# Optimization experiments

Measured on AMD Instinct MI355X. Metric: run time of the kernel, lower is better.

The kernel has to match this reference:

```python
import jax, jax.numpy as jnp
import numpy as np

N_NODES = 100000
N_EDGES = 3200000
IN_DIM, H_DIM, OUT_DIM = 512, 256, 128
NEG_SLOPE = 0.25


def setup_inputs() -> dict:
    key = jax.random.key(0)
    ks = jax.random.split(key, 8)
    x = jax.random.normal(ks[0], (N_NODES, IN_DIM), dtype=jnp.float32)
    # xavier-normal-ish init for weights, zero bias (matches module init)
    W1 = jax.random.normal(ks[1], (IN_DIM, H_DIM), dtype=jnp.float32) * np.sqrt(2.0 / (IN_DIM + H_DIM))
    b1 = jnp.zeros((H_DIM,), dtype=jnp.float32)
    W2 = jax.random.normal(ks[2], (H_DIM, OUT_DIM), dtype=jnp.float32) * np.sqrt(2.0 / (H_DIM + OUT_DIM))
    b2 = jnp.zeros((OUT_DIM,), dtype=jnp.float32)
    adj_row = jax.random.randint(ks[3], (N_EDGES,), 0, N_NODES, dtype=jnp.int32)
    adj_col = jax.random.randint(ks[4], (N_EDGES,), 0, N_NODES, dtype=jnp.int32)
    # positive normalized-ish edge weights (like D^-1/2 A D^-1/2 entries)
    edge_weight = jax.random.uniform(ks[5], (N_EDGES,), dtype=jnp.float32) * 0.05
    return {"x": x, "W1": W1, "b1": b1, "W2": W2, "b2": b2,
            "adj_row": adj_row, "adj_col": adj_col, "edge_weight": edge_weight}


def reference(x, W1, b1, W2, b2, adj_row, adj_col, edge_weight):
    n = x.shape[0]

    def spmm(support):
        # out[r] = sum over edges (r, c): w * support[c]   (COO SpMM)
        msgs = edge_weight[:, None] * support[adj_col]  # [E, d] gather
        return jax.ops.segment_sum(msgs, adj_row, num_segments=n)

    def leaky(h):
        return jnp.where(h > 0, h, NEG_SLOPE * h)

    h = leaky(spmm(x @ W1) + b1)          # gc1 + leaky_relu (dropout = eval mode)
    h = leaky(spmm(h @ W2) + b2)          # gc2 + leaky_relu
    return h
```

## Files before the change

### kernel.cpp

```cpp
#include <hip/hip_runtime.h>

typedef unsigned short u16;
typedef unsigned char u8;
typedef __attribute__((ext_vector_type(8))) __bf16 bf16x8;
typedef __attribute__((ext_vector_type(4))) float f32x4;

#define CAP   4608
#define CAPO  5120
#define CHUNK 8192
#define NBKT_PAD 800
#define NBAND 32

static __device__ __forceinline__ u16 f2bf(float f) {
    unsigned u = __float_as_uint(f);
    u += 0x7fffu + ((u >> 16) & 1u);
    return (u16)(u >> 16);
}
static __device__ __forceinline__ float bf2f(u16 v) {
    return __uint_as_float(((unsigned)v) << 16);
}
static __device__ __forceinline__ void gl_lds16(const void* g, void* l) {
    __builtin_amdgcn_global_load_lds((const __attribute__((address_space(1))) void*)g,
                                     (__attribute__((address_space(3))) void*)l, 16, 0, 0);
}


__global__ __launch_bounds__(256) void bucket_k(const int* __restrict__ row,
                                                const int* __restrict__ col,
                                                const float* __restrict__ w,
                                                int* __restrict__ gcount,
                                                int2* __restrict__ edges, int E) {
    __shared__ int hist[NBKT_PAD];
    __shared__ int lscan[NBKT_PAD];
    __shared__ int lcnt[NBKT_PAD];
    __shared__ int gbase[NBKT_PAD];
    __shared__ int tsum[256];
    __shared__ int2 pay[CHUNK];
    __shared__ int  dst[CHUNK];
    const int base = blockIdx.x * CHUNK;
    const int cntC = min(CHUNK, E - base);
    const int tid = threadIdx.x;

    for (int i = tid; i < NBKT_PAD; i += 256) { hist[i] = 0; lcnt[i] = 0; }
    __syncthreads();

    for (int i = tid; i < cntC; i += 256) atomicAdd(&hist[row[base + i] >> 7], 1);
    __syncthreads();

    int h[4], s = 0;
    #pragma unroll
    for (int j = 0; j < 4; ++j) {
        int bb = tid * 4 + j;
        h[j] = (bb < NBKT_PAD) ? hist[bb] : 0;
        s += h[j];
    }
    tsum[tid] = s;
    __syncthreads();
    for (int d = 1; d < 256; d <<= 1) {
        int t = (tid >= d) ? tsum[tid - d] : 0;
        __syncthreads();
        tsum[tid] += t;
        __syncthreads();
    }
    int run = tsum[tid] - s;
    #pragma unroll
    for (int j = 0; j < 4; ++j) {
        int bb = tid * 4 + j;
        if (bb < NBKT_PAD) {
            lscan[bb] = run;
            run += h[j];
            if (h[j] > 0) gbase[bb] = atomicAdd(&gcount[bb], h[j]);
        }
    }
    __syncthreads();

    for (int i = tid; i < cntC; i += 256) {
        int r = row[base + i];
        int c = col[base + i];
        float ww = w[base + i];
        int bb = r >> 7;
        int lp = atomicAdd(&lcnt[bb], 1);
        int slot = lscan[bb] + lp;
        int pos = gbase[bb] + lp;
        pay[slot] = make_int2(((r & 127) << 17) | c, __float_as_int(ww));
        dst[slot] = (pos < CAP) ? bb * CAP + pos : -1;
    }
    __syncthreads();

    for (int i = tid; i < cntC; i += 256) {
        int d = dst[i];
        if (d >= 0) edges[d] = pay[i];
    }
}


__global__ __launch_bounds__(256) void rsort_k(const int* __restrict__ gcount,
                                               const int2* __restrict__ edges,
                                               int* __restrict__ colsO,
                                               float* __restrict__ wO,
                                               int2* __restrict__ rc, int n) {
    __shared__ int cnt2[128 * NBAND];
    __shared__ int base2[128 * NBAND];
    __shared__ int colsL[CAPO];
    __shared__ float wL[CAPO];
    __shared__ int sc[128];
    const int b = blockIdx.x, tid = threadIdx.x;
    const int cnt = min(gcount[b], CAP);
    const int2* eb = edges + (size_t)b * CAP;

    for (int i = tid; i < 128 * NBAND; i += 256) cnt2[i] = 0;
    for (int i = tid; i < CAPO; i += 256) { colsL[i] = 0; wL[i] = 0.f; }
    __syncthreads();

    for (int i = tid; i < cnt; i += 256) {
        int2 e = eb[i];
        int rr = ((unsigned)e.x) >> 17;
        int cc = e.x & 0x1FFFF;
        atomicAdd(&cnt2[rr * NBAND + (cc >> 12)], 1);
    }
    __syncthreads();

    int rtot = 0;
    if (tid < 128) {
        #pragma unroll
        for (int bb = 0; bb < NBAND; ++bb) rtot += cnt2[tid * NBAND + bb];
        rtot = (rtot + 3) & ~3;
        sc[tid] = rtot;
    }
    __syncthreads();
    for (int d = 1; d < 128; d <<= 1) {
        int t = 0;
        if (tid < 128 && tid >= d) t = sc[tid - d];
        __syncthreads();
        if (tid < 128) sc[tid] += t;
        __syncthreads();
    }
    if (tid < 128) {
        int start = sc[tid] - rtot;
        int gr = b * 128 + tid;
        if (gr < n) rc[gr] = make_int2(b * CAPO + start, rtot);
        int run = start;
        #pragma unroll
        for (int bb = 0; bb < NBAND; ++bb) {
            base2[tid * NBAND + bb] = run;
            run += cnt2[tid * NBAND + bb];
        }
    }
    __syncthreads();

    for (int i = tid; i < cnt; i += 256) {
        int2 e = eb[i];
        int rr = ((unsigned)e.x) >> 17;
        int cc = e.x & 0x1FFFF;
        int slot = atomicAdd(&base2[rr * NBAND + (cc >> 12)], 1);
        colsL[slot] = cc;
        wL[slot] = __int_as_float(e.y);
    }
    __syncthreads();

    int* co = colsO + (size_t)b * CAPO;
    float* wo = wO + (size_t)b * CAPO;
    for (int i = tid; i < CAPO; i += 256) { co[i] = colsL[i]; wo[i] = wL[i]; }
}


__global__ __launch_bounds__(256) void wscale_k(const int* __restrict__ cols,
                                                const float* __restrict__ wr,
                                                const float* __restrict__ scales,
                                                float* __restrict__ ws, int total) {
    int i = (blockIdx.x * 256 + threadIdx.x) * 4;
    const int stride = gridDim.x * 1024;
    for (; i < total; i += stride) {
        int4 c = *(const int4*)(cols + i);
        float4 w = *(const float4*)(wr + i);
        float4 o;
        o.x = w.x * scales[c.x];
        o.y = w.y * scales[c.y];
        o.z = w.z * scales[c.z];
        o.w = w.w * scales[c.w];
        *(float4*)(ws + i) = o;
    }
}


__global__ void transpose_w2(const float* __restrict__ W1, u16* __restrict__ W1T,
                             const float* __restrict__ W2, u16* __restrict__ W2T) {
    const int T1 = 512 * 256;
    const int T2 = 256 * 128;
    int i = blockIdx.x * blockDim.x + threadIdx.x;
    if (i < T1) {
        int k = i / 256, nn = i % 256;
        W1T[nn * 512 + k] = f2bf(W1[i]);
    } else if (i < T1 + T2) {
        int j = i - T1;
        int k = j / 128, nn = j % 128;
        W2T[nn * 256 + k] = f2bf(W2[j]);
    }
}


template <int K, int NWN, bool AF32>
__global__ void gemm_fq(const void* __restrict__ Ap,
                        const u16* __restrict__ BT,
                        u8* __restrict__ supq,
                        float* __restrict__ scales, int M) {
    constexpr int BN = NWN * 64;
    constexpr int THREADS = NWN * 128;
    constexpr int A_ISS = 8192 / (THREADS * 16);
    constexpr int B_ISS = (BN * 64) / (THREADS * 16);
    constexpr int A_CH = 4096 / (THREADS * 8);
    constexpr int LOGN = (NWN == 4) ? 2 : 1;
    __shared__ alignas(16) u16 As[128 * 32];
    __shared__ alignas(16) u16 Bs[BN * 32];
    __shared__ float rmax[128][NWN];
    __shared__ u8 qtile[128 * BN];

    const int tid = threadIdx.x;
    const int lane = tid & 63, wv = tid >> 6;
    const int wm = wv >> LOGN, wn = wv & (NWN - 1);
    const int lr = lane & 15, lg = lane >> 4;
    const int mblk = blockIdx.x;
    f32x4 acc[4][4] = {};
    const float* Af = (const float*)Ap;
    const u16* Ab = (const u16*)Ap;

    const u16* gA[A_ISS > 0 ? A_ISS : 1];
    u16* lA[A_ISS > 0 ? A_ISS : 1];
    const float* gAf[A_CH > 0 ? A_CH : 1];
    u16* lAf[A_CH > 0 ? A_CH : 1];
    if constexpr (AF32) {
        #pragma unroll
        for (int i = 0; i < A_CH; ++i) {
            int t8 = i * THREADS + tid;
            long r = (long)mblk * 128 + (t8 >> 2);
            if (r >= M) r = M - 1;
            gAf[i] = Af + r * K + (t8 & 3) * 8;
            lAf[i] = As + (t8 >> 2) * 32 + (t8 & 3) * 8;
        }
    } else {
        #pragma unroll
        for (int i = 0; i < A_ISS; ++i) {
            int t8 = i * THREADS + tid;
            long r = (long)mblk * 128 + (t8 >> 2);
            if (r >= M) r = M - 1;
            gA[i] = Ab + r * K + (t8 & 3) * 8;
            lA[i] = As + i * THREADS * 8 + wv * 512;
        }
    }
    const u16* gB[B_ISS];
    u16* lB[B_ISS];
    #pragma unroll
    for (int i = 0; i < B_ISS; ++i) {
        int t8 = i * THREADS + tid;
        gB[i] = BT + (long)(t8 >> 2) * K + (t8 & 3) * 8;
        lB[i] = Bs + i * THREADS * 8 + wv * 512;
    }

    #pragma unroll 2
    for (int kt = 0; kt < K; kt += 32) {
        if constexpr (AF32) {
            #pragma unroll
            for (int i = 0; i < A_CH; ++i) {
                float4 f0 = *(const float4*)(gAf[i] + kt);
                float4 f1 = *(const float4*)(gAf[i] + kt + 4);
                alignas(16) u16 t[8];
                t[0] = f2bf(f0.x); t[1] = f2bf(f0.y); t[2] = f2bf(f0.z); t[3] = f2bf(f0.w);
                t[4] = f2bf(f1.x); t[5] = f2bf(f1.y); t[6] = f2bf(f1.z); t[7] = f2bf(f1.w);
                *(int4*)lAf[i] = *(const int4*)t;
            }
        } else {
            #pragma unroll
            for (int i = 0; i < A_ISS; ++i) gl_lds16(gA[i] + kt, lA[i]);
        }
        #pragma unroll
        for (int i = 0; i < B_ISS; ++i) gl_lds16(gB[i] + kt, lB[i]);
        __syncthreads();

        bf16x8 a[4], b[4];
        #pragma unroll
        for (int mi = 0; mi < 4; ++mi)
            a[mi] = *(const bf16x8*)&As[(wm * 64 + mi * 16 + lr) * 32 + lg * 8];
        #pragma unroll
        for (int ni = 0; ni < 4; ++ni)
            b[ni] = *(const bf16x8*)&Bs[(wn * 64 + ni * 16 + lr) * 32 + lg * 8];
        #pragma unroll
        for (int mi = 0; mi < 4; ++mi)
            #pragma unroll
            for (int ni = 0; ni < 4; ++ni)
                acc[mi][ni] = __builtin_amdgcn_mfma_f32_16x16x32_bf16(a[mi], b[ni], acc[mi][ni], 0, 0, 0);
        __syncthreads();
    }

    #pragma unroll
    for (int mi = 0; mi < 4; ++mi) {
        #pragma unroll
        for (int j = 0; j < 4; ++j) {
            float m = 0.f;
            #pragma unroll
            for (int ni = 0; ni < 4; ++ni) m = fmaxf(m, fabsf(acc[mi][ni][j]));
            m = fmaxf(m, __shfl_xor(m, 1));
            m = fmaxf(m, __shfl_xor(m, 2));
            m = fmaxf(m, __shfl_xor(m, 4));
            m = fmaxf(m, __shfl_xor(m, 8));
            if (lr == 0) rmax[wm * 64 + mi * 16 + lg * 4 + j][wn] = m;
        }
    }
    __syncthreads();

    #pragma unroll
    for (int mi = 0; mi < 4; ++mi) {
        #pragma unroll
        for (int j = 0; j < 4; ++j) {
            const int rl = wm * 64 + mi * 16 + lg * 4 + j;
            float m = rmax[rl][0];
            #pragma unroll
            for (int w2 = 1; w2 < NWN; ++w2) m = fmaxf(m, rmax[rl][w2]);
            const float inv = (m > 0.f) ? 127.f / m : 0.f;
            #pragma unroll
            for (int ni = 0; ni < 4; ++ni) {
                int q = (int)rintf(acc[mi][ni][j] * inv) + 128;
                qtile[rl * BN + wn * 64 + ni * 16 + lr] = (u8)q;
            }
        }
    }
    if (tid < 128) {
        int gr = mblk * 128 + tid;
        if (gr < M) {
            float m = rmax[tid][0];
            #pragma unroll
            for (int w2 = 1; w2 < NWN; ++w2) m = fmaxf(m, rmax[tid][w2]);
            scales[gr] = m * (1.f / 127.f);
        }
    }
    __syncthreads();

    constexpr int CHUNKS = (128 * BN) / (THREADS * 16);
    #pragma unroll
    for (int cc = 0; cc < CHUNKS; ++cc) {
        int off = cc * THREADS * 16 + tid * 16;
        int gr = mblk * 128 + off / BN;
        if (gr < M)
            *(int4*)(supq + (size_t)mblk * 128 * BN + off) = *(const int4*)&qtile[off];
    }
}


template <int D, bool OUT_BF16>
__global__ __launch_bounds__(256) void spmm_p(const int2* __restrict__ rc,
                                              const int* __restrict__ cols,
                                              const float* __restrict__ ws,
                                              const u8* __restrict__ supq,
                                              const float* __restrict__ bias,
                                              u16* __restrict__ obf,
                                              float* __restrict__ of32, int n) {
    const int r = blockIdx.x * 4 + (threadIdx.x >> 6);
    if (r >= n) return;
    const int lane = threadIdx.x & 63;
    constexpr int V = D / 64;
    float acc[V];
    #pragma unroll
    for (int j = 0; j < V; ++j) acc[j] = 0.f;
    float kk = 0.f;

    const int2 se = rc[r];
    const int e0  = __builtin_amdgcn_readfirstlane(se.x);
    const int cnt = __builtin_amdgcn_readfirstlane(se.y);
    const int* __restrict__ cp = cols + e0;
    const float* __restrict__ wp = ws + e0;
    const int loff = lane * V;

    #define GATH(dst, c)                                                        \
        if constexpr (V == 4) dst = *(const unsigned*)(supq + (c) * D + loff);  \
        else                  dst = *(const u16*)(supq + (c) * D + loff);

    if (cnt > 0) {
        int4 c0 = *(const int4*)cp;
        float4 w0 = *(const float4*)wp;
        unsigned g0, g1, g2, g3;
        GATH(g0, c0.x); GATH(g1, c0.y); GATH(g2, c0.z); GATH(g3, c0.w);
        int i = 4;
        while (i < cnt) {
            int4 c1 = *(const int4*)(cp + i);
            float4 w1 = *(const float4*)(wp + i);
            unsigned h0, h1, h2, h3;
            GATH(h0, c1.x); GATH(h1, c1.y); GATH(h2, c1.z); GATH(h3, c1.w);
            kk += w0.x + w0.y + w0.z + w0.w;
            acc[0] += w0.x * (float)(g0 & 0xFF) + w0.y * (float)(g1 & 0xFF)
                    + w0.z * (float)(g2 & 0xFF) + w0.w * (float)(g3 & 0xFF);
            acc[1] += w0.x * (float)((g0 >> 8) & 0xFF) + w0.y * (float)((g1 >> 8) & 0xFF)
                    + w0.z * (float)((g2 >> 8) & 0xFF) + w0.w * (float)((g3 >> 8) & 0xFF);
            if constexpr (V == 4) {
                acc[2] += w0.x * (float)((g0 >> 16) & 0xFF) + w0.y * (float)((g1 >> 16) & 0xFF)
                        + w0.z * (float)((g2 >> 16) & 0xFF) + w0.w * (float)((g3 >> 16) & 0xFF);
                acc[3] += w0.x * (float)(g0 >> 24) + w0.y * (float)(g1 >> 24)
                        + w0.z * (float)(g2 >> 24) + w0.w * (float)(g3 >> 24);
            }
            c0 = c1; w0 = w1; g0 = h0; g1 = h1; g2 = h2; g3 = h3;
            i += 4;
        }
        kk += w0.x + w0.y + w0.z + w0.w;
        acc[0] += w0.x * (float)(g0 & 0xFF) + w0.y * (float)(g1 & 0xFF)
                + w0.z * (float)(g2 & 0xFF) + w0.w * (float)(g3 & 0xFF);
        acc[1] += w0.x * (float)((g0 >> 8) & 0xFF) + w0.y * (float)((g1 >> 8) & 0xFF)
                + w0.z * (float)((g2 >> 8) & 0xFF) + w0.w * (float)((g3 >> 8) & 0xFF);
        if constexpr (V == 4) {
            acc[2] += w0.x * (float)((g0 >> 16) & 0xFF) + w0.y * (float)((g1 >> 16) & 0xFF)
                    + w0.z * (float)((g2 >> 16) & 0xFF) + w0.w * (float)((g3 >> 16) & 0xFF);
            acc[3] += w0.x * (float)(g0 >> 24) + w0.y * (float)(g1 >> 24)
                    + w0.z * (float)(g2 >> 24) + w0.w * (float)(g3 >> 24);
        }
    }
    #undef GATH

    const float off = 128.f * kk;
    if constexpr (V == 4) {
        const float4 bb = *(const float4*)&bias[lane * 4];
        float h0 = acc[0] - off + bb.x, h1 = acc[1] - off + bb.y;
        float h2 = acc[2] - off + bb.z, h3 = acc[3] - off + bb.w;
        h0 = h0 > 0.f ? h0 : 0.25f * h0;
        h1 = h1 > 0.f ? h1 : 0.25f * h1;
        h2 = h2 > 0.f ? h2 : 0.25f * h2;
        h3 = h3 > 0.f ? h3 : 0.25f * h3;
        const size_t o = (size_t)r * D + lane * 4;
        if constexpr (OUT_BF16) {
            ushort4 hv; hv.x = f2bf(h0); hv.y = f2bf(h1); hv.z = f2bf(h2); hv.w = f2bf(h3);
            *(ushort4*)&obf[o] = hv;
        } else {
            *(float4*)&of32[o] = make_float4(h0, h1, h2, h3);
        }
    } else {
        const float2 bb = *(const float2*)&bias[lane * 2];
        float h0 = acc[0] - off + bb.x, h1 = acc[1] - off + bb.y;
        h0 = h0 > 0.f ? h0 : 0.25f * h0;
        h1 = h1 > 0.f ? h1 : 0.25f * h1;
        const size_t o = (size_t)r * D + lane * 2;
        if constexpr (OUT_BF16) {
            ushort2 hv; hv.x = f2bf(h0); hv.y = f2bf(h1);
            *(ushort2*)&obf[o] = hv;
        } else {
            *(float2*)&of32[o] = make_float2(h0, h1);
        }
    }
}


extern "C" void kernel_launch(void* const* d_in, const int* in_sizes, int n_in,
                              void* d_out, int out_size, void* d_ws, size_t ws_size,
                              hipStream_t stream) {
    const float* x  = (const float*)d_in[0];
    const float* W1 = (const float*)d_in[1];
    const float* b1 = (const float*)d_in[2];
    const float* W2 = (const float*)d_in[3];
    const float* b2 = (const float*)d_in[4];
    const int* arow = (const int*)d_in[5];
    const int* acol = (const int*)d_in[6];
    const float* ew = (const float*)d_in[7];

    const int IN = 512, H = 256, OUT = 128;
    const int n = in_sizes[0] / IN;
    const int E = in_sizes[5];
    const int nbkt = (n + 127) >> 7;
    const int totS = nbkt * CAPO;

    char* base = (char*)d_ws;
    size_t off = 0;
    auto carve = [&](size_t bytes) -> void* {
        void* r = base + off;
        off = (off + bytes + 255) & ~(size_t)255;
        return r;
    };
    int*   gcount = (int*)carve((size_t)NBKT_PAD * 4);
    int2*  edges  = (int2*)carve((size_t)nbkt * CAP * 8);
    int*   colsS  = (int*)carve((size_t)totS * 4);
    float* wraw   = (float*)carve((size_t)totS * 4);
    float* wsS    = (float*)carve((size_t)totS * 4);
    int2*  rc     = (int2*)carve((size_t)n * 8);
    u16*   W1T    = (u16*)carve((size_t)H * IN * 2);
    u16*   W2T    = (u16*)carve((size_t)OUT * H * 2);
    u8*    supq   = (u8*)carve((size_t)n * H);
    float* scales = (float*)carve((size_t)n * 4);
    u16*   h1     = (u16*)carve((size_t)n * H * 2);

    hipMemsetAsync(gcount, 0, (size_t)NBKT_PAD * 4, stream);
    bucket_k<<<(E + CHUNK - 1) / CHUNK, 256, 0, stream>>>(arow, acol, ew, gcount, edges, E);
    rsort_k<<<nbkt, 256, 0, stream>>>(gcount, edges, colsS, wraw, rc, n);

    transpose_w2<<<(512 * 256 + 256 * 128 + 255) / 256, 256, 0, stream>>>(W1, W1T, W2, W2T);

    gemm_fq<512, 4, true><<<(n + 127) / 128, 512, 0, stream>>>(x, W1T, supq, scales, n);
    wscale_k<<<(totS / 4 + 255) / 256, 256, 0, stream>>>(colsS, wraw, scales, wsS, totS);
    spmm_p<256, true><<<(n + 3) / 4, 256, 0, stream>>>(rc, colsS, wsS, supq, b1, h1, nullptr, n);

    gemm_fq<256, 2, false><<<(n + 127) / 128, 256, 0, stream>>>(h1, W2T, supq, scales, n);
    wscale_k<<<(totS / 4 + 255) / 256, 256, 0, stream>>>(colsS, wraw, scales, wsS, totS);
    spmm_p<128, false><<<(n + 3) / 4, 256, 0, stream>>>(rc, colsS, wsS, supq, b2, nullptr, (float*)d_out, n);
}
```

Baseline: 455.0 us.

## Split SpMM lanes across edges with wider gathers, prefetch GEMM A, fold memset

The SpMM kernels are rewritten so that half-waves (layer 1) or quarter-waves (layer 2) each handle a different edge. Each lane gathers 8 quantized bytes per edge, and the partial sums are combined at the end with cross-lane shuffles. Column indices are stored pre-multiplied by 256, and per-row padding is raised to 8 to match the 8-edge stride. The fp32-A GEMM now register-prefetches the next K tile and uses explicit waitcnt and barriers, and the bucket-counter memset is folded into the weight transpose kernel. These changes aim to raise gather width and memory-level parallelism and to cut launch overhead, at the cost of extra shuffles, a larger padded edge buffer, and 17-bit column shift assumptions.

```diff
diff --git a/kernel.cpp b/kernel.cpp
--- a/kernel.cpp
+++ b/kernel.cpp
@@ -6,18 +6,13 @@
 typedef __attribute__((ext_vector_type(4))) float f32x4;
 
 #define CAP   4608
-#define CAPO  5120
+#define CAPO  5504
 #define CHUNK 8192
 #define NBKT_PAD 800
 #define NBAND 32
 
 static __device__ __forceinline__ u16 f2bf(float f) {
-    unsigned u = __float_as_uint(f);
-    u += 0x7fffu + ((u >> 16) & 1u);
-    return (u16)(u >> 16);
-}
-static __device__ __forceinline__ float bf2f(u16 v) {
-    return __uint_as_float(((unsigned)v) << 16);
+    return __builtin_bit_cast(u16, (__bf16)f);
 }
 static __device__ __forceinline__ void gl_lds16(const void* g, void* l) {
     __builtin_amdgcn_global_load_lds((const __attribute__((address_space(1))) void*)g,
@@ -124,7 +119,7 @@
     if (tid < 128) {
         #pragma unroll
         for (int bb = 0; bb < NBAND; ++bb) rtot += cnt2[tid * NBAND + bb];
-        rtot = (rtot + 3) & ~3;
+        rtot = (rtot + 7) & ~7;
         sc[tid] = rtot;
     }
     __syncthreads();
@@ -153,7 +148,7 @@
         int rr = ((unsigned)e.x) >> 17;
         int cc = e.x & 0x1FFFF;
         int slot = atomicAdd(&base2[rr * NBAND + (cc >> 12)], 1);
-        colsL[slot] = cc;
+        colsL[slot] = cc << 8;
         wL[slot] = __int_as_float(e.y);
     }
     __syncthreads();
@@ -174,20 +169,22 @@
         int4 c = *(const int4*)(cols + i);
         float4 w = *(const float4*)(wr + i);
         float4 o;
-        o.x = w.x * scales[c.x];
-        o.y = w.y * scales[c.y];
-        o.z = w.z * scales[c.z];
-        o.w = w.w * scales[c.w];
+        o.x = w.x * scales[((unsigned)c.x) >> 8];
+        o.y = w.y * scales[((unsigned)c.y) >> 8];
+        o.z = w.z * scales[((unsigned)c.z) >> 8];
+        o.w = w.w * scales[((unsigned)c.w) >> 8];
         *(float4*)(ws + i) = o;
     }
 }
 
 
 __global__ void transpose_w2(const float* __restrict__ W1, u16* __restrict__ W1T,
-                             const float* __restrict__ W2, u16* __restrict__ W2T) {
+                             const float* __restrict__ W2, u16* __restrict__ W2T,
+                             int* __restrict__ gcount) {
     const int T1 = 512 * 256;
     const int T2 = 256 * 128;
     int i = blockIdx.x * blockDim.x + threadIdx.x;
+    if (i < NBKT_PAD) gcount[i] = 0;
     if (i < T1) {
         int k = i / 256, nn = i % 256;
         W1T[nn * 512 + k] = f2bf(W1[i]);
@@ -208,8 +205,8 @@
     constexpr int THREADS = NWN * 128;
     constexpr int A_ISS = 8192 / (THREADS * 16);
     constexpr int B_ISS = (BN * 64) / (THREADS * 16);
-    constexpr int A_CH = 4096 / (THREADS * 8);
     constexpr int LOGN = (NWN == 4) ? 2 : 1;
+    static_assert(!AF32 || (4096 / (THREADS * 8)) == 1, "AF32 path assumes A_CH==1");
     __shared__ alignas(16) u16 As[128 * 32];
     __shared__ alignas(16) u16 Bs[BN * 32];
     __shared__ float rmax[128][NWN];
@@ -224,20 +221,60 @@
     const float* Af = (const float*)Ap;
     const u16* Ab = (const u16*)Ap;
 
-    const u16* gA[A_ISS > 0 ? A_ISS : 1];
-    u16* lA[A_ISS > 0 ? A_ISS : 1];
-    const float* gAf[A_CH > 0 ? A_CH : 1];
-    u16* lAf[A_CH > 0 ? A_CH : 1];
+    const u16* gB[B_ISS];
+    u16* lB[B_ISS];
+    #pragma unroll
+    for (int i = 0; i < B_ISS; ++i) {
+        int t8 = i * THREADS + tid;
+        gB[i] = BT + (long)(t8 >> 2) * K + (t8 & 3) * 8;
+        lB[i] = Bs + i * THREADS * 8 + wv * 512;
+    }
+
     if constexpr (AF32) {
-        #pragma unroll
-        for (int i = 0; i < A_CH; ++i) {
-            int t8 = i * THREADS + tid;
-            long r = (long)mblk * 128 + (t8 >> 2);
-            if (r >= M) r = M - 1;
-            gAf[i] = Af + r * K + (t8 & 3) * 8;
-            lAf[i] = As + (t8 >> 2) * 32 + (t8 & 3) * 8;
+        long r = (long)mblk * 128 + (tid >> 2);
+        if (r >= M) r = M - 1;
+        const float* gAf0 = Af + r * K + (tid & 3) * 8;
+        u16* lAf0 = As + (tid >> 2) * 32 + (tid & 3) * 8;
+
+        float4 pf0 = *(const float4*)(gAf0 + 0);
+        float4 pf1 = *(const float4*)(gAf0 + 4);
+        #pragma unroll 4
+        for (int kt = 0; kt < K; kt += 32) {
+            #pragma unroll
+            for (int i = 0; i < B_ISS; ++i) gl_lds16(gB[i] + kt, lB[i]);
+            __builtin_amdgcn_sched_barrier(0);
+            const int ktn = (kt + 32 < K) ? kt + 32 : 0;
+            float4 nf0 = *(const float4*)(gAf0 + ktn);
+            float4 nf1 = *(const float4*)(gAf0 + ktn + 4);
+            bf16x8 t;
+            t[0] = (__bf16)pf0.x; t[1] = (__bf16)pf0.y; t[2] = (__bf16)pf0.z; t[3] = (__bf16)pf0.w;
+            t[4] = (__bf16)pf1.x; t[5] = (__bf16)pf1.y; t[6] = (__bf16)pf1.z; t[7] = (__bf16)pf1.w;
+            *(bf16x8*)lAf0 = t;
+            asm volatile("s_waitcnt vmcnt(2) lgkmcnt(0)" ::: "memory");
+            __builtin_amdgcn_sched_barrier(0);
+            __builtin_amdgcn_s_barrier();
+            __builtin_amdgcn_sched_barrier(0);
+
+            bf16x8 a[4], b[4];
+            #pragma unroll
+            for (int mi = 0; mi < 4; ++mi)
+                a[mi] = *(const bf16x8*)&As[(wm * 64 + mi * 16 + lr) * 32 + lg * 8];
+            #pragma unroll
+            for (int ni = 0; ni < 4; ++ni)
+                b[ni] = *(const bf16x8*)&Bs[(wn * 64 + ni * 16 + lr) * 32 + lg * 8];
+            #pragma unroll
+            for (int mi = 0; mi < 4; ++mi)
+                #pragma unroll
+                for (int ni = 0; ni < 4; ++ni)
+                    acc[mi][ni] = __builtin_amdgcn_mfma_f32_16x16x32_bf16(a[mi], b[ni], acc[mi][ni], 0, 0, 0);
+            __builtin_amdgcn_sched_barrier(0);
+            __builtin_amdgcn_s_barrier();
+            __builtin_amdgcn_sched_barrier(0);
+            pf0 = nf0; pf1 = nf1;
         }
     } else {
+        const u16* gA[A_ISS];
+        u16* lA[A_ISS];
         #pragma unroll
         for (int i = 0; i < A_ISS; ++i) {
             int t8 = i * THREADS + tid;
@@ -246,49 +283,28 @@
             gA[i] = Ab + r * K + (t8 & 3) * 8;
             lA[i] = As + i * THREADS * 8 + wv * 512;
         }
-    }
-    const u16* gB[B_ISS];
-    u16* lB[B_ISS];
-    #pragma unroll
-    for (int i = 0; i < B_ISS; ++i) {
-        int t8 = i * THREADS + tid;
-        gB[i] = BT + (long)(t8 >> 2) * K + (t8 & 3) * 8;
-        lB[i] = Bs + i * THREADS * 8 + wv * 512;
-    }
-
-    #pragma unroll 2
-    for (int kt = 0; kt < K; kt += 32) {
-        if constexpr (AF32) {
-            #pragma unroll
-            for (int i = 0; i < A_CH; ++i) {
-                float4 f0 = *(const float4*)(gAf[i] + kt);
-                float4 f1 = *(const float4*)(gAf[i] + kt + 4);
-                alignas(16) u16 t[8];
-                t[0] = f2bf(f0.x); t[1] = f2bf(f0.y); t[2] = f2bf(f0.z); t[3] = f2bf(f0.w);
-                t[4] = f2bf(f1.x); t[5] = f2bf(f1.y); t[6] = f2bf(f1.z); t[7] = f2bf(f1.w);
-                *(int4*)lAf[i] = *(const int4*)t;
-            }
-        } else {
+        #pragma unroll 2
+        for (int kt = 0; kt < K; kt += 32) {
             #pragma unroll
             for (int i = 0; i < A_ISS; ++i) gl_lds16(gA[i] + kt, lA[i]);
-        }
-        #pragma unroll
-        for (int i = 0; i < B_ISS; ++i) gl_lds16(gB[i] + kt, lB[i]);
-        __syncthreads();
-
-        bf16x8 a[4], b[4];
-        #pragma unroll
-        for (int mi = 0; mi < 4; ++mi)
-            a[mi] = *(const bf16x8*)&As[(wm * 64 + mi * 16 + lr) * 32 + lg * 8];
-        #pragma unroll
-        for (int ni = 0; ni < 4; ++ni)
-            b[ni] = *(const bf16x8*)&Bs[(wn * 64 + ni * 16 + lr) * 32 + lg * 8];
-        #pragma unroll
-        for (int mi = 0; mi < 4; ++mi)
+            #pragma unroll
+            for (int i = 0; i < B_ISS; ++i) gl_lds16(gB[i] + kt, lB[i]);
+            __syncthreads();
+
+            bf16x8 a[4], b[4];
+            #pragma unroll
+            for (int mi = 0; mi < 4; ++mi)
+                a[mi] = *(const bf16x8*)&As[(wm * 64 + mi * 16 + lr) * 32 + lg * 8];
             #pragma unroll
             for (int ni = 0; ni < 4; ++ni)
-                acc[mi][ni] = __builtin_amdgcn_mfma_f32_16x16x32_bf16(a[mi], b[ni], acc[mi][ni], 0, 0, 0);
-        __syncthreads();
+                b[ni] = *(const bf16x8*)&Bs[(wn * 64 + ni * 16 + lr) * 32 + lg * 8];
+            #pragma unroll
+            for (int mi = 0; mi < 4; ++mi)
+                #pragma unroll
+                for (int ni = 0; ni < 4; ++ni)
+                    acc[mi][ni] = __builtin_amdgcn_mfma_f32_16x16x32_bf16(a[mi], b[ni], acc[mi][ni], 0, 0, 0);
+            __syncthreads();
+        }
     }
 
     #pragma unroll
@@ -345,102 +361,163 @@
 }
 
 
-template <int D, bool OUT_BF16>
-__global__ __launch_bounds__(256) void spmm_p(const int2* __restrict__ rc,
-                                              const int* __restrict__ cols,
-                                              const float* __restrict__ ws,
-                                              const u8* __restrict__ supq,
-                                              const float* __restrict__ bias,
-                                              u16* __restrict__ obf,
-                                              float* __restrict__ of32, int n) {
+__global__ __launch_bounds__(256) void spmm_l1(const int2* __restrict__ rc,
+                                               const int* __restrict__ cols,
+                                               const float* __restrict__ ws,
+                                               const u8* __restrict__ supq,
+                                               const float* __restrict__ bias,
+                                               u16* __restrict__ obf, int n) {
     const int r = blockIdx.x * 4 + (threadIdx.x >> 6);
     if (r >= n) return;
     const int lane = threadIdx.x & 63;
-    constexpr int V = D / 64;
-    float acc[V];
-    #pragma unroll
-    for (int j = 0; j < V; ++j) acc[j] = 0.f;
+    const int half = lane >> 5;
+    const unsigned lsub8 = (unsigned)(lane & 31) * 8;
+    float acc[8] = {0.f, 0.f, 0.f, 0.f, 0.f, 0.f, 0.f, 0.f};
     float kk = 0.f;
-
     const int2 se = rc[r];
     const int e0  = __builtin_amdgcn_readfirstlane(se.x);
     const int cnt = __builtin_amdgcn_readfirstlane(se.y);
     const int* __restrict__ cp = cols + e0;
     const float* __restrict__ wp = ws + e0;
-    const int loff = lane * V;
-
-    #define GATH(dst, c)                                                        \
-        if constexpr (V == 4) dst = *(const unsigned*)(supq + (c) * D + loff);  \
-        else                  dst = *(const u16*)(supq + (c) * D + loff);
+
+#define L1_LOAD(CA, CB, WA, WB, G0, G1, G2, G3, IDX)                                   \
+    CA = *(const int4*)(cp + (IDX));   CB = *(const int4*)(cp + (IDX) + 4);            \
+    WA = *(const float4*)(wp + (IDX)); WB = *(const float4*)(wp + (IDX) + 4);          \
+    G0 = *(const uint2*)(supq + (((unsigned)(half ? CA.y : CA.x)) + lsub8));           \
+    G1 = *(const uint2*)(supq + (((unsigned)(half ? CA.w : CA.z)) + lsub8));           \
+    G2 = *(const uint2*)(supq + (((unsigned)(half ? CB.y : CB.x)) + lsub8));           \
+    G3 = *(const uint2*)(supq + (((unsigned)(half ? CB.w : CB.z)) + lsub8));
+
+#define L1_PAIR(WX, WY, G)                                                              \
+    {   const float wsel = half ? (WY) : (WX);                                          \
+        kk += wsel;                                                                     \
+        acc[0] += wsel * (float)((G).x & 0xFF);                                         \
+        acc[1] += wsel * (float)(((G).x >> 8) & 0xFF);                                  \
+        acc[2] += wsel * (float)(((G).x >> 16) & 0xFF);                                 \
+        acc[3] += wsel * (float)((G).x >> 24);                                          \
+        acc[4] += wsel * (float)((G).y & 0xFF);                                         \
+        acc[5] += wsel * (float)(((G).y >> 8) & 0xFF);                                  \
+        acc[6] += wsel * (float)(((G).y >> 16) & 0xFF);                                 \
+        acc[7] += wsel * (float)((G).y >> 24); }
+
+#define L1_CONS(WA, WB, G0, G1, G2, G3)                                                 \
+    L1_PAIR(WA.x, WA.y, G0) L1_PAIR(WA.z, WA.w, G1)                                     \
+    L1_PAIR(WB.x, WB.y, G2) L1_PAIR(WB.z, WB.w, G3)
 
     if (cnt > 0) {
-        int4 c0 = *(const int4*)cp;
-        float4 w0 = *(const float4*)wp;
-        unsigned g0, g1, g2, g3;
-        GATH(g0, c0.x); GATH(g1, c0.y); GATH(g2, c0.z); GATH(g3, c0.w);
-        int i = 4;
+        int4 ca0, cb0; float4 wa0, wb0; uint2 g0, g1, g2, g3;
+        L1_LOAD(ca0, cb0, wa0, wb0, g0, g1, g2, g3, 0)
+        int i = 8;
         while (i < cnt) {
-            int4 c1 = *(const int4*)(cp + i);
-            float4 w1 = *(const float4*)(wp + i);
-            unsigned h0, h1, h2, h3;
-            GATH(h0, c1.x); GATH(h1, c1.y); GATH(h2, c1.z); GATH(h3, c1.w);
-            kk += w0.x + w0.y + w0.z + w0.w;
-            acc[0] += w0.x * (float)(g0 & 0xFF) + w0.y * (float)(g1 & 0xFF)
-                    + w0.z * (float)(g2 & 0xFF) + w0.w * (float)(g3 & 0xFF);
-            acc[1] += w0.x * (float)((g0 >> 8) & 0xFF) + w0.y * (float)((g1 >> 8) & 0xFF)
-                    + w0.z * (float)((g2 >> 8) & 0xFF) + w0.w * (float)((g3 >> 8) & 0xFF);
-            if constexpr (V == 4) {
-                acc[2] += w0.x * (float)((g0 >> 16) & 0xFF) + w0.y * (float)((g1 >> 16) & 0xFF)
-                        + w0.z * (float)((g2 >> 16) & 0xFF) + w0.w * (float)((g3 >> 16) & 0xFF);
-                acc[3] += w0.x * (float)(g0 >> 24) + w0.y * (float)(g1 >> 24)
-                        + w0.z * (float)(g2 >> 24) + w0.w * (float)(g3 >> 24);
-            }
-            c0 = c1; w0 = w1; g0 = h0; g1 = h1; g2 = h2; g3 = h3;
-            i += 4;
-        }
-        kk += w0.x + w0.y + w0.z + w0.w;
-        acc[0] += w0.x * (float)(g0 & 0xFF) + w0.y * (float)(g1 & 0xFF)
-                + w0.z * (float)(g2 & 0xFF) + w0.w * (float)(g3 & 0xFF);
-        acc[1] += w0.x * (float)((g0 >> 8) & 0xFF) + w0.y * (float)((g1 >> 8) & 0xFF)
-                + w0.z * (float)((g2 >> 8) & 0xFF) + w0.w * (float)((g3 >> 8) & 0xFF);
-        if constexpr (V == 4) {
-            acc[2] += w0.x * (float)((g0 >> 16) & 0xFF) + w0.y * (float)((g1 >> 16) & 0xFF)
-                    + w0.z * (float)((g2 >> 16) & 0xFF) + w0.w * (float)((g3 >> 16) & 0xFF);
-            acc[3] += w0.x * (float)(g0 >> 24) + w0.y * (float)(g1 >> 24)
-                    + w0.z * (float)(g2 >> 24) + w0.w * (float)(g3 >> 24);
-        }
-    }
-    #undef GATH
+            int4 ca1, cb1; float4 wa1, wb1; uint2 h0, h1, h2, h3;
+            L1_LOAD(ca1, cb1, wa1, wb1, h0, h1, h2, h3, i)
+            L1_CONS(wa0, wb0, g0, g1, g2, g3)
+            wa0 = wa1; wb0 = wb1; g0 = h0; g1 = h1; g2 = h2; g3 = h3;
+            i += 8;
+        }
+        L1_CONS(wa0, wb0, g0, g1, g2, g3)
+    }
+#undef L1_LOAD
+#undef L1_PAIR
+#undef L1_CONS
+
+    kk += __shfl_xor(kk, 32);
+    #pragma unroll
+    for (int j = 0; j < 8; ++j) acc[j] += __shfl_xor(acc[j], 32);
 
     const float off = 128.f * kk;
-    if constexpr (V == 4) {
-        const float4 bb = *(const float4*)&bias[lane * 4];
-        float h0 = acc[0] - off + bb.x, h1 = acc[1] - off + bb.y;
-        float h2 = acc[2] - off + bb.z, h3 = acc[3] - off + bb.w;
-        h0 = h0 > 0.f ? h0 : 0.25f * h0;
-        h1 = h1 > 0.f ? h1 : 0.25f * h1;
-        h2 = h2 > 0.f ? h2 : 0.25f * h2;
-        h3 = h3 > 0.f ? h3 : 0.25f * h3;
-        const size_t o = (size_t)r * D + lane * 4;
-        if constexpr (OUT_BF16) {
-            ushort4 hv; hv.x = f2bf(h0); hv.y = f2bf(h1); hv.z = f2bf(h2); hv.w = f2bf(h3);
-            *(ushort4*)&obf[o] = hv;
-        } else {
-            *(float4*)&of32[o] = make_float4(h0, h1, h2, h3);
-        }
-    } else {
-        const float2 bb = *(const float2*)&bias[lane * 2];
-        float h0 = acc[0] - off + bb.x, h1 = acc[1] - off + bb.y;
-        h0 = h0 > 0.f ? h0 : 0.25f * h0;
-        h1 = h1 > 0.f ? h1 : 0.25f * h1;
-        const size_t o = (size_t)r * D + lane * 2;
-        if constexpr (OUT_BF16) {
-            ushort2 hv; hv.x = f2bf(h0); hv.y = f2bf(h1);
-            *(ushort2*)&obf[o] = hv;
-        } else {
-            *(float2*)&of32[o] = make_float2(h0, h1);
-        }
-    }
+    float a0 = half ? acc[4] : acc[0];
+    float a1 = half ? acc[5] : acc[1];
+    float a2 = half ? acc[6] : acc[2];
+    float a3 = half ? acc[7] : acc[3];
+    const int d0 = (lane & 31) * 8 + half * 4;
+    const float4 bb = *(const float4*)&bias[d0];
+    float h0 = a0 - off + bb.x, h1 = a1 - off + bb.y;
+    float h2 = a2 - off + bb.z, h3 = a3 - off + bb.w;
+    h0 = h0 > 0.f ? h0 : 0.25f * h0;
+    h1 = h1 > 0.f ? h1 : 0.25f * h1;
+    h2 = h2 > 0.f ? h2 : 0.25f * h2;
+    h3 = h3 > 0.f ? h3 : 0.25f * h3;
+    ushort4 hv; hv.x = f2bf(h0); hv.y = f2bf(h1); hv.z = f2bf(h2); hv.w = f2bf(h3);
+    *(ushort4*)&obf[(size_t)r * 256 + d0] = hv;
+}
+
+
+__global__ __launch_bounds__(256) void spmm_l2(const int2* __restrict__ rc,
+                                               const int* __restrict__ cols,
+                                               const float* __restrict__ ws,
+                                               const u8* __restrict__ supq,
+                                               const float* __restrict__ bias,
+                                               float* __restrict__ of32, int n) {
+    const int r = blockIdx.x * 4 + (threadIdx.x >> 6);
+    if (r >= n) return;
+    const int lane = threadIdx.x & 63;
+    const int quad = lane >> 4;
+    const unsigned lsub8 = (unsigned)(lane & 15) * 8;
+    float acc[8] = {0.f, 0.f, 0.f, 0.f, 0.f, 0.f, 0.f, 0.f};
+    float kk = 0.f;
+    const int2 se = rc[r];
+    const int e0  = __builtin_amdgcn_readfirstlane(se.x);
+    const int cnt = __builtin_amdgcn_readfirstlane(se.y);
+    const int* __restrict__ cp = cols + e0;
+    const float* __restrict__ wp = ws + e0;
+
+#define L2_SELI(CA) ((quad & 2) ? ((quad & 1) ? (CA).w : (CA).z) : ((quad & 1) ? (CA).y : (CA).x))
+#define L2_SELF(WA) ((quad & 2) ? ((quad & 1) ? (WA).w : (WA).z) : ((quad & 1) ? (WA).y : (WA).x))
+
+#define L2_LOAD(CA, CB, WA, WB, G0, G1, IDX)                                           \
+    CA = *(const int4*)(cp + (IDX));   CB = *(const int4*)(cp + (IDX) + 4);            \
+    WA = *(const float4*)(wp + (IDX)); WB = *(const float4*)(wp + (IDX) + 4);          \
+    G0 = *(const uint2*)(supq + ((((unsigned)L2_SELI(CA)) >> 1) + lsub8));             \
+    G1 = *(const uint2*)(supq + ((((unsigned)L2_SELI(CB)) >> 1) + lsub8));
+
+#define L2_QUAD(WA, G)                                                                  \
+    {   const float wsel = L2_SELF(WA);                                                 \
+        kk += wsel;                                                                     \
+        acc[0] += wsel * (float)((G).x & 0xFF);                                         \
+        acc[1] += wsel * (float)(((G).x >> 8) & 0xFF);                                  \
+        acc[2] += wsel * (float)(((G).x >> 16) & 0xFF);                                 \
+        acc[3] += wsel * (float)((G).x >> 24);                                          \
+        acc[4] += wsel * (float)((G).y & 0xFF);                                         \
+        acc[5] += wsel * (float)(((G).y >> 8) & 0xFF);                                  \
+        acc[6] += wsel * (float)(((G).y >> 16) & 0xFF);                                 \
+        acc[7] += wsel * (float)((G).y >> 24); }
+
+    if (cnt > 0) {
+        int4 ca0, cb0; float4 wa0, wb0; uint2 g0, g1;
+        L2_LOAD(ca0, cb0, wa0, wb0, g0, g1, 0)
+        int i = 8;
+        while (i < cnt) {
+            int4 ca1, cb1; float4 wa1, wb1; uint2 h0, h1;
+            L2_LOAD(ca1, cb1, wa1, wb1, h0, h1, i)
+            L2_QUAD(wa0, g0) L2_QUAD(wb0, g1)
+            wa0 = wa1; wb0 = wb1; g0 = h0; g1 = h1;
+            i += 8;
+        }
+        L2_QUAD(wa0, g0) L2_QUAD(wb0, g1)
+    }
+#undef L2_LOAD
+#undef L2_QUAD
+#undef L2_SELI
+#undef L2_SELF
+
+    kk += __shfl_xor(kk, 16);
+    kk += __shfl_xor(kk, 32);
+    #pragma unroll
+    for (int j = 0; j < 8; ++j) {
+        acc[j] += __shfl_xor(acc[j], 16);
+        acc[j] += __shfl_xor(acc[j], 32);
+    }
+
+    const float off = 128.f * kk;
+    float a0 = (quad & 2) ? ((quad & 1) ? acc[6] : acc[4]) : ((quad & 1) ? acc[2] : acc[0]);
+    float a1 = (quad & 2) ? ((quad & 1) ? acc[7] : acc[5]) : ((quad & 1) ? acc[3] : acc[1]);
+    const int d0 = (lane & 15) * 8 + quad * 2;
+    const float2 bb = *(const float2*)&bias[d0];
+    float h0 = a0 - off + bb.x, h1 = a1 - off + bb.y;
+    h0 = h0 > 0.f ? h0 : 0.25f * h0;
+    h1 = h1 > 0.f ? h1 : 0.25f * h1;
+    *(float2*)&of32[(size_t)r * 128 + d0] = make_float2(h0, h1);
 }
 
 
@@ -481,17 +558,16 @@
     float* scales = (float*)carve((size_t)n * 4);
     u16*   h1     = (u16*)carve((size_t)n * H * 2);
 
-    hipMemsetAsync(gcount, 0, (size_t)NBKT_PAD * 4, stream);
+    transpose_w2<<<(512 * 256 + 256 * 128 + 255) / 256, 256, 0, stream>>>(W1, W1T, W2, W2T, gcount);
+
     bucket_k<<<(E + CHUNK - 1) / CHUNK, 256, 0, stream>>>(arow, acol, ew, gcount, edges, E);
     rsort_k<<<nbkt, 256, 0, stream>>>(gcount, edges, colsS, wraw, rc, n);
 
-    transpose_w2<<<(512 * 256 + 256 * 128 + 255) / 256, 256, 0, stream>>>(W1, W1T, W2, W2T);
-
     gemm_fq<512, 4, true><<<(n + 127) / 128, 512, 0, stream>>>(x, W1T, supq, scales, n);
     wscale_k<<<(totS / 4 + 255) / 256, 256, 0, stream>>>(colsS, wraw, scales, wsS, totS);
-    spmm_p<256, true><<<(n + 3) / 4, 256, 0, stream>>>(rc, colsS, wsS, supq, b1, h1, nullptr, n);
+    spmm_l1<<<(n + 3) / 4, 256, 0, stream>>>(rc, colsS, wsS, supq, b1, h1, n);
 
     gemm_fq<256, 2, false><<<(n + 127) / 128, 256, 0, stream>>>(h1, W2T, supq, scales, n);
     wscale_k<<<(totS / 4 + 255) / 256, 256, 0, stream>>>(colsS, wraw, scales, wsS, totS);
-    spmm_p<128, false><<<(n + 3) / 4, 256, 0, stream>>>(rc, colsS, wsS, supq, b2, nullptr, (float*)d_out, n);
-}
+    spmm_l2<<<(n + 3) / 4, 256, 0, stream>>>(rc, colsS, wsS, supq, b2, (float*)d_out, n);
+}
```

New measurement: 437.5 us (median of 3 runs). -3.8%, faster.
